# Kernel optimization log

Measured on AMD Instinct MI355X. Metric: run time of the kernel, lower is better.

The kernel has to match this reference:

```python
import jax, jax.numpy as jnp
import numpy as np

DIM, E, H, HS = 2048, 8, 1408, 2816
B, S = 4, 2048


def setup_inputs() -> dict:
    key = jax.random.key(0)
    ks = jax.random.split(key, 12)
    sc = 0.02
    return {
        "x": jax.random.normal(ks[0], (B, S, DIM), jnp.float32),
        "gate_w": jax.random.normal(ks[1], (E, DIM), jnp.float32) * sc,
        "gate_b": jnp.zeros((E,), jnp.float32),
        "w1": jax.random.normal(ks[2], (E, H, DIM), jnp.float32) * sc,
        "b1": jnp.zeros((E, H), jnp.float32),
        "w3": jax.random.normal(ks[3], (E, H, DIM), jnp.float32) * sc,
        "b3": jnp.zeros((E, H), jnp.float32),
        "w2": jax.random.normal(ks[4], (E, DIM, H), jnp.float32) * sc,
        "b2": jnp.zeros((E, DIM), jnp.float32),
        "sh_gate": jax.random.normal(ks[5], (HS, DIM), jnp.float32) * sc,
        "sh_up": jax.random.normal(ks[6], (HS, DIM), jnp.float32) * sc,
        "sh_down": jax.random.normal(ks[7], (DIM, HS), jnp.float32) * sc,
        "top_k": 2,
    }


def reference(x, gate_w, gate_b, w1, b1, w3, b3, w2, b2, sh_gate, sh_up, sh_down, top_k):
    shape = x.shape
    xt = x.reshape(-1, DIM)                       # [T, D]
    T = xt.shape[0]

    # Router: softmax -> top-k (bias is None so gathered weights == topk probs)
    logits = xt @ gate_w.T + gate_b               # [T, E]
    scores = jax.nn.softmax(logits, axis=-1)
    topk_w, topk_idx = jax.lax.top_k(scores, top_k)  # [T, K]
    # combine weights per (token, expert); topk indices are distinct per row
    combine = jnp.zeros((T, E), xt.dtype).at[jnp.arange(T)[:, None], topk_idx].add(topk_w)

    # Routed experts: dense batched SwiGLU over all experts, weighted combine.
    g = jax.nn.silu(jnp.einsum("td,ehd->teh", xt, w1) + b1)  # [T, E, H]
    u = jnp.einsum("td,ehd->teh", xt, w3) + b3               # [T, E, H]
    hw = (g * u) * combine[:, :, None]                        # weight before down-proj
    routed = jnp.einsum("teh,edh->td", hw, w2) + combine @ b2  # [T, D]

    # Shared expert (bias-free SwiGLU)
    shared = (jax.nn.silu(xt @ sh_gate.T) * (xt @ sh_up.T)) @ sh_down.T

    return (shared + routed).reshape(shape)
```

## Files before the change

### kernel.cpp

```cpp
#include <hip/hip_runtime.h>
#include <stdint.h>

#define DIM  2048
#define NEXP 8
#define NH   1408
#define NHS  2816
#define NT   8192
#define NA   (NT*2)

typedef unsigned short u16;
typedef short bf16x8 __attribute__((ext_vector_type(8)));
typedef float f32x4 __attribute__((ext_vector_type(4)));

typedef __attribute__((address_space(1))) const uint32_t gas_u32;
typedef __attribute__((address_space(3))) uint32_t las_u32;

__device__ __forceinline__ u16 f2bf(float f) {
  uint32_t x = __builtin_bit_cast(uint32_t, f);
  x += 0x7FFFu + ((x >> 16) & 1u);
  return (u16)(x >> 16);
}

__device__ __forceinline__ void gload_lds16(const void* g, void* l) {
  __builtin_amdgcn_global_load_lds((gas_u32*)g, (las_u32*)l, 16, 0, 0);
}

struct alignas(16) US8 { u16 u[8]; };

__global__ __launch_bounds__(256) void convert_kernel(const float* __restrict__ src,
                                                      u16* __restrict__ dst, int n8) {
  int i = blockIdx.x * 256 + threadIdx.x;
  if (i >= n8) return;
  const float4* s = (const float4*)src + (size_t)i * 2;
  float4 a = s[0], b = s[1];
  US8 r;
  r.u[0]=f2bf(a.x); r.u[1]=f2bf(a.y); r.u[2]=f2bf(a.z); r.u[3]=f2bf(a.w);
  r.u[4]=f2bf(b.x); r.u[5]=f2bf(b.y); r.u[6]=f2bf(b.z); r.u[7]=f2bf(b.w);
  *((US8*)dst + i) = r;
}

__global__ void zero_counts(int* counts) { if (threadIdx.x < NEXP) counts[threadIdx.x] = 0; }

__global__ __launch_bounds__(64) void router_kernel(const float* __restrict__ x,
    const float* __restrict__ gw, const float* __restrict__ gb,
    int* __restrict__ tope, float* __restrict__ topw, int* __restrict__ counts) {
  const int t = blockIdx.x;
  const int lane = threadIdx.x;
  const float4* xr = (const float4*)(x + (size_t)t * DIM);
  float4 xv[8];
  #pragma unroll
  for (int j = 0; j < 8; j++) xv[j] = xr[j * 64 + lane];
  float p[NEXP];
  #pragma unroll
  for (int e = 0; e < NEXP; e++) {
    const float4* gr = (const float4*)(gw + (size_t)e * DIM);
    float s = 0.f;
    #pragma unroll
    for (int j = 0; j < 8; j++) {
      float4 g = gr[j * 64 + lane];
      s += xv[j].x*g.x + xv[j].y*g.y + xv[j].z*g.z + xv[j].w*g.w;
    }
    p[e] = s;
  }
  #pragma unroll
  for (int off = 32; off > 0; off >>= 1) {
    #pragma unroll
    for (int e = 0; e < NEXP; e++) p[e] += __shfl_xor(p[e], off);
  }
  if (lane == 0) {
    float pr[NEXP];
    float mx = -1e30f;
    #pragma unroll
    for (int e = 0; e < NEXP; e++) { p[e] += gb[e]; mx = fmaxf(mx, p[e]); }
    float den = 0.f;
    #pragma unroll
    for (int e = 0; e < NEXP; e++) { pr[e] = __expf(p[e] - mx); den += pr[e]; }
    float inv = 1.f / den;
    #pragma unroll
    for (int e = 0; e < NEXP; e++) pr[e] *= inv;
    int e0 = 0;
    #pragma unroll
    for (int e = 1; e < NEXP; e++) if (pr[e] > pr[e0]) e0 = e;
    int e1 = (e0 == 0) ? 1 : 0;
    #pragma unroll
    for (int e = 0; e < NEXP; e++) { if (e != e0 && pr[e] > pr[e1]) e1 = e; }
    tope[t*2]   = e0; tope[t*2+1] = e1;
    topw[t*2]   = pr[e0]; topw[t*2+1] = pr[e1];
    atomicAdd(&counts[e0], 1); atomicAdd(&counts[e1], 1);
  }
}

__global__ void scan_kernel(const int* __restrict__ counts, int* __restrict__ offsets,
                            int* __restrict__ cursor) {
  if (threadIdx.x == 0) {
    int s = 0;
    for (int e = 0; e < NEXP; e++) { offsets[e] = s; cursor[e] = s; s += counts[e]; }
    offsets[NEXP] = s;
  }
}

__global__ __launch_bounds__(256) void assign_kernel(const int* __restrict__ tope,
    const float* __restrict__ topw, int* __restrict__ cursor,
    int* __restrict__ ptok, float* __restrict__ pw) {
  int t = blockIdx.x * 256 + threadIdx.x;
  if (t >= NT) return;
  #pragma unroll
  for (int k = 0; k < 2; k++) {
    int e = tope[t*2+k];
    int pos = atomicAdd(&cursor[e], 1);
    ptok[pos] = t;
    pw[pos]   = topw[t*2+k];
  }
}

template<bool ROUTED>
__global__ __launch_bounds__(256, 2) void gemm_up(
    const u16* __restrict__ X,
    const u16* __restrict__ Wg,
    const u16* __restrict__ Wu,
    const float* __restrict__ Bg,
    const float* __restrict__ Bu,
    u16* __restrict__ Hout,
    const int* __restrict__ offsets,
    const int* __restrict__ ptok,
    const float* __restrict__ pw,
    int Nfeat)
{
  const int nt = blockIdx.x;
  const int mt = blockIdx.y;
  int e = 0, seg = 0, cnt = NT;
  if (ROUTED) {
    e = blockIdx.z;
    seg = offsets[e];
    cnt = offsets[e+1] - seg;
    if (mt * 128 >= cnt) return;
  }
  const int m0 = mt * 128;
  const int tid = threadIdx.x;
  const int wave = tid >> 6, lane = tid & 63;

  __shared__ u16 sA[128*32];
  __shared__ u16 sBg[64*32];
  __shared__ u16 sBu[64*32];
  char* sAc  = (char*)sA;
  char* sBgc = (char*)sBg;
  char* sBuc = (char*)sBu;

  const u16* aSrc[2];
  #pragma unroll
  for (int j = 0; j < 2; j++) {
    int c = j * 256 + tid;
    int row = c >> 2, pos = c & 3;
    int gch = pos ^ (row & 3);
    int r = m0 + row;
    size_t srow;
    if (ROUTED) { r = (r < cnt) ? r : (cnt - 1); srow = (size_t)ptok[seg + r]; }
    else        { srow = (size_t)r; }
    aSrc[j] = X + srow * DIM + gch * 8;
  }
  const size_t wOff = ROUTED ? (size_t)e * Nfeat * DIM : 0;
  {
  }
  const int brow = tid >> 2, bpos = tid & 3;
  const int bgch = bpos ^ (brow & 3);
  const u16* bgSrc = Wg + wOff + (size_t)(nt * 64 + brow) * DIM + bgch * 8;
  const u16* buSrc = Wu + wOff + (size_t)(nt * 64 + brow) * DIM + bgch * 8;

  f32x4 accg[4][2], accu[4][2];
  #pragma unroll
  for (int m = 0; m < 4; m++)
    #pragma unroll
    for (int n = 0; n < 2; n++) { accg[m][n] = (f32x4){0,0,0,0}; accu[m][n] = (f32x4){0,0,0,0}; }

  const int wr = (wave >> 1) * 64;
  const int wc = (wave & 1) * 32;
  const int lr = lane & 15, kg = lane >> 4;
  int aOff[4], bOff[2];
  #pragma unroll
  for (int m = 0; m < 4; m++) { int row = wr + m*16 + lr; aOff[m] = row*64 + ((kg ^ (row & 3)) * 16); }
  #pragma unroll
  for (int n = 0; n < 2; n++) { int row = wc + n*16 + lr; bOff[n] = row*64 + ((kg ^ (row & 3)) * 16); }

  const int ldsA0 = wave * 1024, ldsA1 = 4096 + wave * 1024, ldsB = wave * 1024;

  for (int k0 = 0; k0 < DIM; k0 += 32) {
    __syncthreads();
    gload_lds16(aSrc[0] + k0, sAc  + ldsA0);
    gload_lds16(aSrc[1] + k0, sAc  + ldsA1);
    gload_lds16(bgSrc  + k0, sBgc + ldsB);
    gload_lds16(buSrc  + k0, sBuc + ldsB);
    __syncthreads();
    bf16x8 af[4], bgf[2], buf2[2];
    #pragma unroll
    for (int m = 0; m < 4; m++) af[m] = *(const bf16x8*)(sAc + aOff[m]);
    #pragma unroll
    for (int n = 0; n < 2; n++) {
      bgf[n]  = *(const bf16x8*)(sBgc + bOff[n]);
      buf2[n] = *(const bf16x8*)(sBuc + bOff[n]);
    }
    #pragma unroll
    for (int m = 0; m < 4; m++)
      #pragma unroll
      for (int n = 0; n < 2; n++) {
        accg[m][n] = __builtin_amdgcn_mfma_f32_16x16x32_bf16(af[m], bgf[n],  accg[m][n], 0, 0, 0);
        accu[m][n] = __builtin_amdgcn_mfma_f32_16x16x32_bf16(af[m], buf2[n], accu[m][n], 0, 0, 0);
      }
  }

  const int col0 = nt * 64 + wc;
  #pragma unroll
  for (int m = 0; m < 4; m++) {
    #pragma unroll
    for (int n = 0; n < 2; n++) {
      #pragma unroll
      for (int i = 0; i < 4; i++) {
        int rl = wr + m*16 + (lane >> 4) * 4 + i;
        int gr = m0 + rl;
        if (ROUTED && gr >= cnt) continue;
        int col = col0 + n*16 + (lane & 15);
        float g = accg[m][n][i];
        float u = accu[m][n][i];
        float scale = 1.f;
        size_t orow;
        if (ROUTED) {
          int ai = seg + gr;
          scale = pw[ai];
          g += Bg[e * Nfeat + col];
          u += Bu[e * Nfeat + col];
          orow = (size_t)ai;
        } else {
          orow = (size_t)gr;
        }
        float s = g / (1.f + __expf(-g));
        Hout[orow * (size_t)Nfeat + col] = f2bf(s * u * scale);
      }
    }
  }
}

template<bool ROUTED>
__global__ __launch_bounds__(256, 2) void gemm_down(
    const u16* __restrict__ Hin,
    const u16* __restrict__ W,
    const float* __restrict__ B2,
    float* __restrict__ Out,
    const int* __restrict__ offsets,
    const int* __restrict__ ptok,
    const float* __restrict__ pw,
    int Kdim)
{
  const int nt = blockIdx.x;
  const int mt = blockIdx.y;
  int e = 0, seg = 0, cnt = NT;
  if (ROUTED) {
    e = blockIdx.z;
    seg = offsets[e];
    cnt = offsets[e+1] - seg;
    if (mt * 128 >= cnt) return;
  }
  const int m0 = mt * 128;
  const int tid = threadIdx.x;
  const int wave = tid >> 6, lane = tid & 63;

  __shared__ u16 sA[128*32];
  __shared__ u16 sB[128*32];
  char* sAc = (char*)sA;
  char* sBc = (char*)sB;

  const u16* aSrc[2]; const u16* bSrc[2];
  #pragma unroll
  for (int j = 0; j < 2; j++) {
    int c = j * 256 + tid;
    int row = c >> 2, pos = c & 3;
    int gch = pos ^ (row & 3);
    int r = m0 + row;
    size_t arow;
    if (ROUTED) { r = (r < cnt) ? r : (cnt - 1); arow = (size_t)(seg + r); }
    else        { arow = (size_t)r; }
    aSrc[j] = Hin + arow * (size_t)Kdim + gch * 8;
    size_t brow = (size_t)(ROUTED ? e * DIM : 0) + nt * 128 + row;
    bSrc[j] = W + brow * (size_t)Kdim + gch * 8;
  }

  f32x4 acc[4][4];
  #pragma unroll
  for (int m = 0; m < 4; m++)
    #pragma unroll
    for (int n = 0; n < 4; n++) acc[m][n] = (f32x4){0,0,0,0};

  const int wr = (wave >> 1) * 64, wc = (wave & 1) * 64;
  const int lr = lane & 15, kg = lane >> 4;
  int aOff[4], bOff[4];
  #pragma unroll
  for (int m = 0; m < 4; m++) { int row = wr + m*16 + lr; aOff[m] = row*64 + ((kg ^ (row & 3)) * 16); }
  #pragma unroll
  for (int n = 0; n < 4; n++) { int row = wc + n*16 + lr; bOff[n] = row*64 + ((kg ^ (row & 3)) * 16); }

  for (int k0 = 0; k0 < Kdim; k0 += 32) {
    __syncthreads();
    gload_lds16(aSrc[0] + k0, sAc + wave * 1024);
    gload_lds16(aSrc[1] + k0, sAc + 4096 + wave * 1024);
    gload_lds16(bSrc[0] + k0, sBc + wave * 1024);
    gload_lds16(bSrc[1] + k0, sBc + 4096 + wave * 1024);
    __syncthreads();
    bf16x8 af[4], bf[4];
    #pragma unroll
    for (int m = 0; m < 4; m++) af[m] = *(const bf16x8*)(sAc + aOff[m]);
    #pragma unroll
    for (int n = 0; n < 4; n++) bf[n] = *(const bf16x8*)(sBc + bOff[n]);
    #pragma unroll
    for (int m = 0; m < 4; m++)
      #pragma unroll
      for (int n = 0; n < 4; n++)
        acc[m][n] = __builtin_amdgcn_mfma_f32_16x16x32_bf16(af[m], bf[n], acc[m][n], 0, 0, 0);
  }

  const int col0 = nt * 128 + wc;
  #pragma unroll
  for (int m = 0; m < 4; m++) {
    #pragma unroll
    for (int n = 0; n < 4; n++) {
      #pragma unroll
      for (int i = 0; i < 4; i++) {
        int rl = wr + m*16 + (lane >> 4) * 4 + i;
        int gr = m0 + rl;
        int col = col0 + n*16 + (lane & 15);
        float v = acc[m][n][i];
        if (ROUTED) {
          if (gr < cnt) {
            int ai = seg + gr;
            int token = ptok[ai];
            float w = pw[ai];
            atomicAdd(Out + (size_t)token * DIM + col, v + w * B2[e * DIM + col]);
          }
        } else {
          Out[(size_t)gr * DIM + col] = v;
        }
      }
    }
  }
}

extern "C" void kernel_launch(void* const* d_in, const int* in_sizes, int n_in,
                              void* d_out, int out_size, void* d_ws, size_t ws_size,
                              hipStream_t stream) {
  (void)in_sizes; (void)n_in; (void)out_size; (void)ws_size;
  const float* x      = (const float*)d_in[0];
  const float* gate_w = (const float*)d_in[1];
  const float* gate_b = (const float*)d_in[2];
  const float* w1     = (const float*)d_in[3];
  const float* b1     = (const float*)d_in[4];
  const float* w3     = (const float*)d_in[5];
  const float* b3     = (const float*)d_in[6];
  const float* w2     = (const float*)d_in[7];
  const float* b2     = (const float*)d_in[8];
  const float* shg    = (const float*)d_in[9];
  const float* shu    = (const float*)d_in[10];
  const float* shd    = (const float*)d_in[11];
  float* out = (float*)d_out;

  char* ws = (char*)d_ws;
  size_t off = 0;
  auto alloc = [&](size_t bytes) -> void* {
    void* p = ws + off;
    off += (bytes + 255) & ~(size_t)255;
    return p;
  };
  u16* xb    = (u16*)alloc((size_t)NT * DIM * 2);
  u16* w1b   = (u16*)alloc((size_t)NEXP * NH * DIM * 2);
  u16* w3b   = (u16*)alloc((size_t)NEXP * NH * DIM * 2);
  u16* w2b   = (u16*)alloc((size_t)NEXP * DIM * NH * 2);
  u16* shgb  = (u16*)alloc((size_t)NHS * DIM * 2);
  u16* shub  = (u16*)alloc((size_t)NHS * DIM * 2);
  u16* shdb  = (u16*)alloc((size_t)DIM * NHS * 2);
  u16* hsh   = (u16*)alloc((size_t)NT * NHS * 2);
  u16* hr    = (u16*)alloc((size_t)NA * NH * 2);
  int*   tope    = (int*)alloc(NT * 2 * 4);
  float* topw    = (float*)alloc(NT * 2 * 4);
  int*   ptok    = (int*)alloc(NA * 4);
  float* pw      = (float*)alloc(NA * 4);
  int*   counts  = (int*)alloc(64);
  int*   offsets = (int*)alloc(64);
  int*   cursor  = (int*)alloc(64);

  auto cvt = [&](const float* s, u16* d, size_t n) {
    int n8 = (int)(n / 8);
    convert_kernel<<<(n8 + 255) / 256, 256, 0, stream>>>(s, d, n8);
  };
  cvt(x,   xb,   (size_t)NT * DIM);
  cvt(w1,  w1b,  (size_t)NEXP * NH * DIM);
  cvt(w3,  w3b,  (size_t)NEXP * NH * DIM);
  cvt(w2,  w2b,  (size_t)NEXP * DIM * NH);
  cvt(shg, shgb, (size_t)NHS * DIM);
  cvt(shu, shub, (size_t)NHS * DIM);
  cvt(shd, shdb, (size_t)DIM * NHS);

  zero_counts<<<1, 64, 0, stream>>>(counts);
  router_kernel<<<NT, 64, 0, stream>>>(x, gate_w, gate_b, tope, topw, counts);
  scan_kernel<<<1, 1, 0, stream>>>(counts, offsets, cursor);
  assign_kernel<<<NT / 256, 256, 0, stream>>>(tope, topw, cursor, ptok, pw);

  gemm_up<false><<<dim3(NHS / 64, NT / 128, 1), 256, 0, stream>>>(
      xb, shgb, shub, nullptr, nullptr, hsh, nullptr, nullptr, nullptr, NHS);
  gemm_up<true><<<dim3(NH / 64, NT / 128, NEXP), 256, 0, stream>>>(
      xb, w1b, w3b, b1, b3, hr, offsets, ptok, pw, NH);
  gemm_down<false><<<dim3(DIM / 128, NT / 128, 1), 256, 0, stream>>>(
      hsh, shdb, nullptr, out, nullptr, nullptr, nullptr, NHS);
  gemm_down<true><<<dim3(DIM / 128, NT / 128, NEXP), 256, 0, stream>>>(
      hr, w2b, b2, out, offsets, ptok, pw, NH);
}
```

Before: 1.265 ms.

## Replace GEMMs with 256x256 double-buffered 8-wave kernel and interleaved gate/up weights

Replaces the separate up/down GEMM kernels with one templated 256x256-tile, 512-thread kernel. It uses 128KB of dynamic LDS, double-buffered K=64 stages, phased MFMA with setprio, and a tile-swizzled launch order. Gate and up weights are converted into a row-interleaved layout so one B operand covers both, and the SwiGLU pairs are joined with a lane shuffle in the epilogue. This aims to raise arithmetic intensity and overlap global loads with MFMA work. The cost is heavy LDS use and wasted work on padded routed tiles. The 2048/64 and 1408/64 K loops run an even number of stages, which the two-stages-per-iteration loop needs.

```diff
diff --git a/kernel.cpp b/kernel.cpp
--- a/kernel.cpp
+++ b/kernel.cpp
@@ -37,6 +37,19 @@
   r.u[0]=f2bf(a.x); r.u[1]=f2bf(a.y); r.u[2]=f2bf(a.z); r.u[3]=f2bf(a.w);
   r.u[4]=f2bf(b.x); r.u[5]=f2bf(b.y); r.u[6]=f2bf(b.z); r.u[7]=f2bf(b.w);
   *((US8*)dst + i) = r;
+}
+
+__global__ __launch_bounds__(256) void convert_ilv(const float* __restrict__ src,
+                                                   u16* __restrict__ dst, int n8, int par) {
+  int i = blockIdx.x * 256 + threadIdx.x;
+  if (i >= n8) return;
+  int row = i >> 8, c = i & 255;
+  const float4* s = (const float4*)src + (size_t)i * 2;
+  float4 a = s[0], b = s[1];
+  US8 r;
+  r.u[0]=f2bf(a.x); r.u[1]=f2bf(a.y); r.u[2]=f2bf(a.z); r.u[3]=f2bf(a.w);
+  r.u[4]=f2bf(b.x); r.u[5]=f2bf(b.y); r.u[6]=f2bf(b.z); r.u[7]=f2bf(b.w);
+  *((US8*)dst + (((size_t)(2*row + par)) << 8) + c) = r;
 }
 
 __global__ void zero_counts(int* counts) { if (threadIdx.x < NEXP) counts[threadIdx.x] = 0; }
@@ -113,232 +126,196 @@
   }
 }
 
-template<bool ROUTED>
-__global__ __launch_bounds__(256, 2) void gemm_up(
-    const u16* __restrict__ X,
-    const u16* __restrict__ Wg,
-    const u16* __restrict__ Wu,
-    const float* __restrict__ Bg,
-    const float* __restrict__ Bu,
-    u16* __restrict__ Hout,
-    const int* __restrict__ offsets,
-    const int* __restrict__ ptok,
+#define BARRIER() { asm volatile("" ::: "memory"); __builtin_amdgcn_s_barrier(); asm volatile("" ::: "memory"); }
+#define LGKM0    asm volatile("s_waitcnt lgkmcnt(0)" ::: "memory")
+#define VMCNT4   asm volatile("s_waitcnt vmcnt(4)" ::: "memory")
+
+template<int EPI>
+__global__ __launch_bounds__(512, 2) void gemm8(
+    const u16* __restrict__ A, const u16* __restrict__ Bw,
+    void* __restrict__ OutV,
+    const float* __restrict__ biasG, const float* __restrict__ biasU,
+    const int* __restrict__ offsets, const int* __restrict__ ptok,
     const float* __restrict__ pw,
-    int Nfeat)
+    int M, int N, int K, int Hf)
 {
-  const int nt = blockIdx.x;
-  const int mt = blockIdx.y;
-  int e = 0, seg = 0, cnt = NT;
-  if (ROUTED) {
-    e = blockIdx.z;
-    seg = offsets[e];
-    cnt = offsets[e+1] - seg;
-    if (mt * 128 >= cnt) return;
-  }
-  const int m0 = mt * 128;
-  const int tid = threadIdx.x;
-  const int wave = tid >> 6, lane = tid & 63;
-
-  __shared__ u16 sA[128*32];
-  __shared__ u16 sBg[64*32];
-  __shared__ u16 sBu[64*32];
-  char* sAc  = (char*)sA;
-  char* sBgc = (char*)sBg;
-  char* sBuc = (char*)sBu;
-
-  const u16* aSrc[2];
+  constexpr bool SEG = (EPI==1)||(EPI==3);
+  extern __shared__ char smem[];
+  const int gx = gridDim.x;
+  const int nwg = gx * gridDim.y;
+  const int f = blockIdx.y * gx + blockIdx.x;
+  const int swz = (f & 7) * (nwg >> 3) + (f >> 3);
+  const int nt = swz % gx, mt = swz / gx;
+  int e = 0, seg = 0, cnt = M;
+  if (SEG) {
+    e = blockIdx.z; seg = offsets[e]; cnt = offsets[e+1] - seg;
+    if (mt*256 >= cnt) return;
+  }
+  const int tid = threadIdx.x, wave = tid>>6, lane = tid&63;
+  const int NKT = K >> 6;
+
+  const u16* Bp = Bw + (SEG ? (size_t)e * (size_t)N * K : (size_t)0);
+  const u16* sA[2][2]; const u16* sB[2][2];
+  {
+    const int trow = tid >> 3;
+    const int tch  = (tid & 7) ^ (trow & 7);
+    #pragma unroll
+    for (int h = 0; h < 2; h++)
+      #pragma unroll
+      for (int j = 0; j < 2; j++) {
+        int r = mt*256 + h*128 + j*64 + trow;
+        if (SEG) r = (r < cnt) ? r : (cnt - 1);
+        size_t arow;
+        if (EPI == 1)      arow = (size_t)ptok[seg + r];
+        else if (EPI == 3) arow = (size_t)(seg + r);
+        else               arow = (size_t)r;
+        sA[h][j] = A + arow * (size_t)K + tch*8;
+        int br = nt*256 + h*128 + j*64 + trow;
+        sB[h][j] = Bp + (size_t)br * K + tch*8;
+      }
+  }
+
+  const int wm = wave>>2, wn = wave&3, hb = wn>>1;
+  const int ln15 = lane & 15, kg = lane >> 4;
+  const int c0 = ((kg ^ (ln15 & 7)) << 4);
+  const char* A0 = smem + (wm<<14);
+  const char* A1 = smem + ((2+wm)<<14);
+  const char* B0c = smem + 65536 + (hb<<14);
+  const char* B1c = smem + 65536 + ((2+hb)<<14);
+  const int arow0 = ln15*128;
+  const int brow0 = ((wn&1)*64 + ln15)*128;
+
+  f32x4 acc[8][4];
   #pragma unroll
-  for (int j = 0; j < 2; j++) {
-    int c = j * 256 + tid;
-    int row = c >> 2, pos = c & 3;
-    int gch = pos ^ (row & 3);
-    int r = m0 + row;
-    size_t srow;
-    if (ROUTED) { r = (r < cnt) ? r : (cnt - 1); srow = (size_t)ptok[seg + r]; }
-    else        { srow = (size_t)r; }
-    aSrc[j] = X + srow * DIM + gch * 8;
-  }
-  const size_t wOff = ROUTED ? (size_t)e * Nfeat * DIM : 0;
-  {
-  }
-  const int brow = tid >> 2, bpos = tid & 3;
-  const int bgch = bpos ^ (brow & 3);
-  const u16* bgSrc = Wg + wOff + (size_t)(nt * 64 + brow) * DIM + bgch * 8;
-  const u16* buSrc = Wu + wOff + (size_t)(nt * 64 + brow) * DIM + bgch * 8;
-
-  f32x4 accg[4][2], accu[4][2];
-  #pragma unroll
-  for (int m = 0; m < 4; m++)
-    #pragma unroll
-    for (int n = 0; n < 2; n++) { accg[m][n] = (f32x4){0,0,0,0}; accu[m][n] = (f32x4){0,0,0,0}; }
-
-  const int wr = (wave >> 1) * 64;
-  const int wc = (wave & 1) * 32;
-  const int lr = lane & 15, kg = lane >> 4;
-  int aOff[4], bOff[2];
-  #pragma unroll
-  for (int m = 0; m < 4; m++) { int row = wr + m*16 + lr; aOff[m] = row*64 + ((kg ^ (row & 3)) * 16); }
-  #pragma unroll
-  for (int n = 0; n < 2; n++) { int row = wc + n*16 + lr; bOff[n] = row*64 + ((kg ^ (row & 3)) * 16); }
-
-  const int ldsA0 = wave * 1024, ldsA1 = 4096 + wave * 1024, ldsB = wave * 1024;
-
-  for (int k0 = 0; k0 < DIM; k0 += 32) {
-    __syncthreads();
-    gload_lds16(aSrc[0] + k0, sAc  + ldsA0);
-    gload_lds16(aSrc[1] + k0, sAc  + ldsA1);
-    gload_lds16(bgSrc  + k0, sBgc + ldsB);
-    gload_lds16(buSrc  + k0, sBuc + ldsB);
-    __syncthreads();
-    bf16x8 af[4], bgf[2], buf2[2];
-    #pragma unroll
-    for (int m = 0; m < 4; m++) af[m] = *(const bf16x8*)(sAc + aOff[m]);
-    #pragma unroll
-    for (int n = 0; n < 2; n++) {
-      bgf[n]  = *(const bf16x8*)(sBgc + bOff[n]);
-      buf2[n] = *(const bf16x8*)(sBuc + bOff[n]);
-    }
-    #pragma unroll
-    for (int m = 0; m < 4; m++)
+  for (int m = 0; m < 8; m++)
+    #pragma unroll
+    for (int n = 0; n < 4; n++) acc[m][n] = (f32x4){0,0,0,0};
+
+  bf16x8 fa[4][2], fbl[2][2], fbh[2][2];
+
+#define STA(b, h, kt) { int kc = (kt); kc = (kc < NKT-1) ? kc : (NKT-1); \
+  gload_lds16(sA[h][0] + kc*64, smem + (((b)*2+(h))<<14) + wave*1024); \
+  gload_lds16(sA[h][1] + kc*64, smem + (((b)*2+(h))<<14) + 8192 + wave*1024); }
+#define STB(b, h, kt) { int kc = (kt); kc = (kc < NKT-1) ? kc : (NKT-1); \
+  gload_lds16(sB[h][0] + kc*64, smem + 65536 + (((b)*2+(h))<<14) + wave*1024); \
+  gload_lds16(sB[h][1] + kc*64, smem + 65536 + (((b)*2+(h))<<14) + 8192 + wave*1024); }
+#define LD_FA(BASE, HI) { _Pragma("unroll") for (int m = 0; m < 4; m++) { \
+  const char* p_ = (BASE) + ((HI)*4+m)*2048 + arow0; \
+  fa[m][0] = *(const bf16x8*)(p_ + c0); fa[m][1] = *(const bf16x8*)(p_ + (c0^64)); } }
+#define LD_FB(BASE, HI, FB) { _Pragma("unroll") for (int n = 0; n < 2; n++) { \
+  const char* p_ = (BASE) + ((HI)*2+n)*2048 + brow0; \
+  FB[n][0] = *(const bf16x8*)(p_ + c0); FB[n][1] = *(const bf16x8*)(p_ + (c0^64)); } }
+#define PH_MFMA(MI0, NI0, FB) { __builtin_amdgcn_s_setprio(1); \
+  _Pragma("unroll") for (int kk = 0; kk < 2; kk++) \
+  _Pragma("unroll") for (int m = 0; m < 4; m++) \
+  _Pragma("unroll") for (int n = 0; n < 2; n++) \
+    acc[(MI0)+m][(NI0)+n] = __builtin_amdgcn_mfma_f32_16x16x32_bf16(fa[m][kk], FB[n][kk], acc[(MI0)+m][(NI0)+n], 0, 0, 0); \
+  __builtin_amdgcn_s_setprio(0); }
+
+  STB(0,0,0); STB(0,1,0); STA(0,0,0); STA(0,1,0); STB(1,0,1); STB(1,1,1);
+  VMCNT4; BARRIER();
+
+  for (int t = 0; t < NKT; t += 2) {
+    LD_FA(A0, 0); LD_FB(B0c, 0, fbl);
+    STA(1, 0, t+1);
+    BARRIER(); LGKM0;
+    PH_MFMA(0, 0, fbl);
+    BARRIER();
+    LD_FB(B0c, 1, fbh);
+    STA(1, 1, t+1);
+    BARRIER(); LGKM0;
+    PH_MFMA(0, 2, fbh);
+    BARRIER();
+    LD_FA(A0, 1);
+    STB(0, 0, t+2);
+    BARRIER(); LGKM0;
+    PH_MFMA(4, 2, fbh);
+    BARRIER();
+    STB(0, 1, t+2);
+    VMCNT4;
+    BARRIER(); LGKM0;
+    PH_MFMA(4, 0, fbl);
+    BARRIER();
+    LD_FA(A1, 0); LD_FB(B1c, 0, fbl);
+    STA(0, 0, t+2);
+    BARRIER(); LGKM0;
+    PH_MFMA(0, 0, fbl);
+    BARRIER();
+    LD_FB(B1c, 1, fbh);
+    STA(0, 1, t+2);
+    BARRIER(); LGKM0;
+    PH_MFMA(0, 2, fbh);
+    BARRIER();
+    LD_FA(A1, 1);
+    STB(1, 0, t+3);
+    BARRIER(); LGKM0;
+    PH_MFMA(4, 2, fbh);
+    BARRIER();
+    STB(1, 1, t+3);
+    VMCNT4;
+    BARRIER(); LGKM0;
+    PH_MFMA(4, 0, fbl);
+    BARRIER();
+  }
+
+  if (EPI == 0 || EPI == 1) {
+    u16* Hout = (u16*)OutV;
+    #pragma unroll
+    for (int mi = 0; mi < 8; mi++) {
       #pragma unroll
-      for (int n = 0; n < 2; n++) {
-        accg[m][n] = __builtin_amdgcn_mfma_f32_16x16x32_bf16(af[m], bgf[n],  accg[m][n], 0, 0, 0);
-        accu[m][n] = __builtin_amdgcn_mfma_f32_16x16x32_bf16(af[m], buf2[n], accu[m][n], 0, 0, 0);
-      }
-  }
-
-  const int col0 = nt * 64 + wc;
-  #pragma unroll
-  for (int m = 0; m < 4; m++) {
-    #pragma unroll
-    for (int n = 0; n < 2; n++) {
-      #pragma unroll
-      for (int i = 0; i < 4; i++) {
-        int rl = wr + m*16 + (lane >> 4) * 4 + i;
-        int gr = m0 + rl;
-        if (ROUTED && gr >= cnt) continue;
-        int col = col0 + n*16 + (lane & 15);
-        float g = accg[m][n][i];
-        float u = accu[m][n][i];
-        float scale = 1.f;
-        size_t orow;
-        if (ROUTED) {
-          int ai = seg + gr;
-          scale = pw[ai];
-          g += Bg[e * Nfeat + col];
-          u += Bu[e * Nfeat + col];
-          orow = (size_t)ai;
-        } else {
-          orow = (size_t)gr;
-        }
-        float s = g / (1.f + __expf(-g));
-        Hout[orow * (size_t)Nfeat + col] = f2bf(s * u * scale);
-      }
-    }
-  }
-}
-
-template<bool ROUTED>
-__global__ __launch_bounds__(256, 2) void gemm_down(
-    const u16* __restrict__ Hin,
-    const u16* __restrict__ W,
-    const float* __restrict__ B2,
-    float* __restrict__ Out,
-    const int* __restrict__ offsets,
-    const int* __restrict__ ptok,
-    const float* __restrict__ pw,
-    int Kdim)
-{
-  const int nt = blockIdx.x;
-  const int mt = blockIdx.y;
-  int e = 0, seg = 0, cnt = NT;
-  if (ROUTED) {
-    e = blockIdx.z;
-    seg = offsets[e];
-    cnt = offsets[e+1] - seg;
-    if (mt * 128 >= cnt) return;
-  }
-  const int m0 = mt * 128;
-  const int tid = threadIdx.x;
-  const int wave = tid >> 6, lane = tid & 63;
-
-  __shared__ u16 sA[128*32];
-  __shared__ u16 sB[128*32];
-  char* sAc = (char*)sA;
-  char* sBc = (char*)sB;
-
-  const u16* aSrc[2]; const u16* bSrc[2];
-  #pragma unroll
-  for (int j = 0; j < 2; j++) {
-    int c = j * 256 + tid;
-    int row = c >> 2, pos = c & 3;
-    int gch = pos ^ (row & 3);
-    int r = m0 + row;
-    size_t arow;
-    if (ROUTED) { r = (r < cnt) ? r : (cnt - 1); arow = (size_t)(seg + r); }
-    else        { arow = (size_t)r; }
-    aSrc[j] = Hin + arow * (size_t)Kdim + gch * 8;
-    size_t brow = (size_t)(ROUTED ? e * DIM : 0) + nt * 128 + row;
-    bSrc[j] = W + brow * (size_t)Kdim + gch * 8;
-  }
-
-  f32x4 acc[4][4];
-  #pragma unroll
-  for (int m = 0; m < 4; m++)
-    #pragma unroll
-    for (int n = 0; n < 4; n++) acc[m][n] = (f32x4){0,0,0,0};
-
-  const int wr = (wave >> 1) * 64, wc = (wave & 1) * 64;
-  const int lr = lane & 15, kg = lane >> 4;
-  int aOff[4], bOff[4];
-  #pragma unroll
-  for (int m = 0; m < 4; m++) { int row = wr + m*16 + lr; aOff[m] = row*64 + ((kg ^ (row & 3)) * 16); }
-  #pragma unroll
-  for (int n = 0; n < 4; n++) { int row = wc + n*16 + lr; bOff[n] = row*64 + ((kg ^ (row & 3)) * 16); }
-
-  for (int k0 = 0; k0 < Kdim; k0 += 32) {
-    __syncthreads();
-    gload_lds16(aSrc[0] + k0, sAc + wave * 1024);
-    gload_lds16(aSrc[1] + k0, sAc + 4096 + wave * 1024);
-    gload_lds16(bSrc[0] + k0, sBc + wave * 1024);
-    gload_lds16(bSrc[1] + k0, sBc + 4096 + wave * 1024);
-    __syncthreads();
-    bf16x8 af[4], bf[4];
-    #pragma unroll
-    for (int m = 0; m < 4; m++) af[m] = *(const bf16x8*)(sAc + aOff[m]);
-    #pragma unroll
-    for (int n = 0; n < 4; n++) bf[n] = *(const bf16x8*)(sBc + bOff[n]);
-    #pragma unroll
-    for (int m = 0; m < 4; m++)
-      #pragma unroll
-      for (int n = 0; n < 4; n++)
-        acc[m][n] = __builtin_amdgcn_mfma_f32_16x16x32_bf16(af[m], bf[n], acc[m][n], 0, 0, 0);
-  }
-
-  const int col0 = nt * 128 + wc;
-  #pragma unroll
-  for (int m = 0; m < 4; m++) {
-    #pragma unroll
-    for (int n = 0; n < 4; n++) {
-      #pragma unroll
-      for (int i = 0; i < 4; i++) {
-        int rl = wr + m*16 + (lane >> 4) * 4 + i;
-        int gr = m0 + rl;
-        int col = col0 + n*16 + (lane & 15);
-        float v = acc[m][n][i];
-        if (ROUTED) {
-          if (gr < cnt) {
-            int ai = seg + gr;
-            int token = ptok[ai];
-            float w = pw[ai];
-            atomicAdd(Out + (size_t)token * DIM + col, v + w * B2[e * DIM + col]);
+      for (int ni = 0; ni < 4; ni++) {
+        int colC = nt*256 + wn*64 + ni*16 + ln15;
+        int h = colC >> 1;
+        int par = ln15 & 1;
+        #pragma unroll
+        for (int i = 0; i < 4; i++) {
+          float v = acc[mi][ni][i];
+          float v2 = __shfl_xor(v, 1);
+          float g = par ? v2 : v;
+          float uu = par ? v : v2;
+          int rr = mt*256 + wm*128 + mi*16 + kg*4 + i;
+          if (EPI == 1) { g += biasG[e*Hf + h]; uu += biasU[e*Hf + h]; }
+          float hv = (g / (1.f + __expf(-g))) * uu;
+          if (EPI == 0) {
+            if (par == 0) Hout[(size_t)rr * Hf + h] = f2bf(hv);
+          } else {
+            if (par == 0 && rr < cnt) {
+              int ai = seg + rr;
+              Hout[(size_t)ai * Hf + h] = f2bf(hv * pw[ai]);
+            }
           }
-        } else {
-          Out[(size_t)gr * DIM + col] = v;
         }
       }
     }
-  }
+  } else {
+    float* Out = (float*)OutV;
+    #pragma unroll
+    for (int mi = 0; mi < 8; mi++) {
+      #pragma unroll
+      for (int ni = 0; ni < 4; ni++) {
+        int col = nt*256 + wn*64 + ni*16 + ln15;
+        #pragma unroll
+        for (int i = 0; i < 4; i++) {
+          int rr = mt*256 + wm*128 + mi*16 + kg*4 + i;
+          float v = acc[mi][ni][i];
+          if (EPI == 2) {
+            Out[(size_t)rr * DIM + col] = v;
+          } else {
+            if (rr < cnt) {
+              int ai = seg + rr;
+              int token = ptok[ai];
+              atomicAdd(Out + (size_t)token * DIM + col, v + pw[ai] * biasG[e*DIM + col]);
+            }
+          }
+        }
+      }
+    }
+  }
+#undef STA
+#undef STB
+#undef LD_FA
+#undef LD_FB
+#undef PH_MFMA
 }
 
 extern "C" void kernel_launch(void* const* d_in, const int* in_sizes, int n_in,
@@ -367,11 +344,9 @@
     return p;
   };
   u16* xb    = (u16*)alloc((size_t)NT * DIM * 2);
-  u16* w1b   = (u16*)alloc((size_t)NEXP * NH * DIM * 2);
-  u16* w3b   = (u16*)alloc((size_t)NEXP * NH * DIM * 2);
+  u16* wupr  = (u16*)alloc((size_t)NEXP * 2 * NH * DIM * 2);
   u16* w2b   = (u16*)alloc((size_t)NEXP * DIM * NH * 2);
-  u16* shgb  = (u16*)alloc((size_t)NHS * DIM * 2);
-  u16* shub  = (u16*)alloc((size_t)NHS * DIM * 2);
+  u16* wupsh = (u16*)alloc((size_t)2 * NHS * DIM * 2);
   u16* shdb  = (u16*)alloc((size_t)DIM * NHS * 2);
   u16* hsh   = (u16*)alloc((size_t)NT * NHS * 2);
   u16* hr    = (u16*)alloc((size_t)NA * NH * 2);
@@ -383,16 +358,28 @@
   int*   offsets = (int*)alloc(64);
   int*   cursor  = (int*)alloc(64);
 
+  {
+    auto setA = [](const void* fp) {
+      (void)hipFuncSetAttribute(fp, hipFuncAttributeMaxDynamicSharedMemorySize, 131072);
+    };
+    setA((const void*)gemm8<0>); setA((const void*)gemm8<1>);
+    setA((const void*)gemm8<2>); setA((const void*)gemm8<3>);
+  }
+
   auto cvt = [&](const float* s, u16* d, size_t n) {
     int n8 = (int)(n / 8);
     convert_kernel<<<(n8 + 255) / 256, 256, 0, stream>>>(s, d, n8);
   };
+  auto cvi = [&](const float* s, u16* d, size_t n, int par) {
+    int n8 = (int)(n / 8);
+    convert_ilv<<<(n8 + 255) / 256, 256, 0, stream>>>(s, d, n8, par);
+  };
   cvt(x,   xb,   (size_t)NT * DIM);
-  cvt(w1,  w1b,  (size_t)NEXP * NH * DIM);
-  cvt(w3,  w3b,  (size_t)NEXP * NH * DIM);
+  cvi(w1,  wupr, (size_t)NEXP * NH * DIM, 0);
+  cvi(w3,  wupr, (size_t)NEXP * NH * DIM, 1);
   cvt(w2,  w2b,  (size_t)NEXP * DIM * NH);
-  cvt(shg, shgb, (size_t)NHS * DIM);
-  cvt(shu, shub, (size_t)NHS * DIM);
+  cvi(shg, wupsh, (size_t)NHS * DIM, 0);
+  cvi(shu, wupsh, (size_t)NHS * DIM, 1);
   cvt(shd, shdb, (size_t)DIM * NHS);
 
   zero_counts<<<1, 64, 0, stream>>>(counts);
@@ -400,12 +387,16 @@
   scan_kernel<<<1, 1, 0, stream>>>(counts, offsets, cursor);
   assign_kernel<<<NT / 256, 256, 0, stream>>>(tope, topw, cursor, ptok, pw);
 
-  gemm_up<false><<<dim3(NHS / 64, NT / 128, 1), 256, 0, stream>>>(
-      xb, shgb, shub, nullptr, nullptr, hsh, nullptr, nullptr, nullptr, NHS);
-  gemm_up<true><<<dim3(NH / 64, NT / 128, NEXP), 256, 0, stream>>>(
-      xb, w1b, w3b, b1, b3, hr, offsets, ptok, pw, NH);
-  gemm_down<false><<<dim3(DIM / 128, NT / 128, 1), 256, 0, stream>>>(
-      hsh, shdb, nullptr, out, nullptr, nullptr, nullptr, NHS);
-  gemm_down<true><<<dim3(DIM / 128, NT / 128, NEXP), 256, 0, stream>>>(
-      hr, w2b, b2, out, offsets, ptok, pw, NH);
-}
+  gemm8<0><<<dim3(2*NHS/256, NT/256, 1), 512, 131072, stream>>>(
+      xb, wupsh, hsh, nullptr, nullptr, nullptr, nullptr, nullptr,
+      NT, 2*NHS, DIM, NHS);
+  gemm8<1><<<dim3(2*NH/256, NT/256, NEXP), 512, 131072, stream>>>(
+      xb, wupr, hr, b1, b3, offsets, ptok, pw,
+      NT, 2*NH, DIM, NH);
+  gemm8<2><<<dim3(DIM/256, NT/256, 1), 512, 131072, stream>>>(
+      hsh, shdb, out, nullptr, nullptr, nullptr, nullptr, nullptr,
+      NT, DIM, NHS, 0);
+  gemm8<3><<<dim3(DIM/256, NT/256, NEXP), 512, 131072, stream>>>(
+      hr, w2b, out, b2, nullptr, offsets, ptok, pw,
+      NT, DIM, NH, 0);
+}
```

Result: slower. 2.185 ms (+72.8%).
